# Optimization experiments

Measured on AMD Instinct MI355X. Metric: run time of the kernel, lower is better.

The kernel has to match this reference:

```python
import jax, jax.numpy as jnp
import numpy as np

B, C, D, H, W = 8, 16, 32, 112, 112
D_OUT, H3, W3, H2, W2 = 16, 14, 14, 7, 7
HID, OUT = 256, 128
IN_SIZE = C * H2 * W2  # 784


def setup_inputs() -> dict:
    key = jax.random.key(0)
    ks = jax.random.split(key, 8)
    s_ih = 1.0 / np.sqrt(HID)
    return {
        "x": jax.random.normal(ks[0], (B, C, D, H, W), dtype=jnp.float32),
        "W_ih": jax.random.uniform(ks[1], (3 * HID, IN_SIZE), jnp.float32, -s_ih, s_ih),
        "W_hh": jax.random.uniform(ks[2], (3 * HID, HID), jnp.float32, -s_ih, s_ih),
        "b_ih": jax.random.uniform(ks[3], (3 * HID,), jnp.float32, -s_ih, s_ih),
        "b_hh": jax.random.uniform(ks[4], (3 * HID,), jnp.float32, -s_ih, s_ih),
        "W_out": jax.random.uniform(ks[5], (OUT, HID), jnp.float32, -s_ih, s_ih),
        "b_out": jax.random.uniform(ks[6], (OUT,), jnp.float32, -s_ih, s_ih),
    }


def reference(x, W_ih, W_hh, b_ih, b_hh, W_out, b_out):
    # AdaptiveAvgPool3d (D,H,W)->(D_OUT,H3,W3): divisible factors -> mean pooling
    p3 = x.reshape(B, C, D_OUT, D // D_OUT, H3, H // H3, W3, W // W3).mean(axis=(3, 5, 7))
    # AdaptiveAvgPool2d per temporal slice (H3,W3)->(H2,W2)
    p2 = p3.reshape(B, C, D_OUT, H2, H3 // H2, W2, W3 // W2).mean(axis=(4, 6))
    # sequence over D_OUT: [T, B, C*H2*W2]
    seq = p2.transpose(2, 0, 1, 3, 4).reshape(D_OUT, B, IN_SIZE)

    def step(h, inp):
        gi = inp @ W_ih.T + b_ih  # [B, 3H]
        gh = h @ W_hh.T + b_hh    # [B, 3H]
        ir, iz, inn = jnp.split(gi, 3, axis=-1)
        hr, hz, hn = jnp.split(gh, 3, axis=-1)
        r = jax.nn.sigmoid(ir + hr)
        z = jax.nn.sigmoid(iz + hz)
        n = jnp.tanh(inn + r * hn)
        h_new = (1.0 - z) * n + z * h
        return h_new, None

    h0 = jnp.zeros((B, HID), dtype=x.dtype)
    h, _ = jax.lax.scan(step, h0, seq)
    return h @ W_out.T + b_out
```

## Files before the change

kernel.cpp:

```cpp
#include <hip/hip_runtime.h>
#include <hip/hip_bf16.h>
#include <cstdint>

#define BB 8
#define CC 16
#define DD 32
#define HH 112
#define WW 112
#define TT 16
#define HID 256
#define OUTN 128
#define INSZ 784
#define NCACHE 48
#define NTAIL (128 - NCACHE)

typedef _Float16 h2v __attribute__((ext_vector_type(2)));

__device__ __forceinline__ float bf16lo(uint32_t u) { return __uint_as_float(u << 16); }
__device__ __forceinline__ float bf16hi(uint32_t u) { return __uint_as_float(u & 0xffff0000u); }
__device__ __forceinline__ float bf16s(uint16_t u)  { return __uint_as_float(((uint32_t)u) << 16); }

__device__ __forceinline__ uint16_t f32_to_bf16_rne(float f) {
    uint32_t u = __float_as_uint(f);
    return (uint16_t)((u + 0x7fffu + ((u >> 16) & 1u)) >> 16);
}

__device__ __forceinline__ float dot2f(uint32_t w, uint32_t h, float acc) {
#if __has_builtin(__builtin_amdgcn_fdot2)
    return __builtin_amdgcn_fdot2(__builtin_bit_cast(h2v, w),
                                  __builtin_bit_cast(h2v, h), acc, false);
#else
    h2v wv = __builtin_bit_cast(h2v, w), hv = __builtin_bit_cast(h2v, h);
    return acc + (float)wv.x * (float)hv.x + (float)wv.y * (float)hv.y;
#endif
}

__global__ __launch_bounds__(256) void detect_kernel(const uint16_t* __restrict__ x,
                                                     int* __restrict__ flag) {
    __shared__ int cnt;
    if (threadIdx.x == 0) cnt = 0;
    __syncthreads();
    int local = 0;
    for (int i = threadIdx.x; i < 8192; i += 256) {
        uint32_t e = (x[i] >> 7) & 0xFFu;
        if (e == 0u || e >= 0x90u) local++;
    }
    atomicAdd(&cnt, local);
    __syncthreads();
    if (threadIdx.x == 0) *flag = (cnt > 400) ? 1 : 0;
}

__global__ __launch_bounds__(256) void pool_kernel(const void* __restrict__ xv,
                                                   float* __restrict__ seq,
                                                   const int* __restrict__ flag) {
    const int isf32 = *flag;
    int gid = blockIdx.x;
    int t = gid & 15, c = (gid >> 4) & 15, b = gid >> 8;
    long base = (long)(((b * CC + c) * DD) + t * 2) * (HH * WW);
    __shared__ float chunk[6272];
    int tid = threadIdx.x;
    float s = 0.0f;
    if (!isf32) {
        const uint4* p = reinterpret_cast<const uint4*>((const uint16_t*)xv + base);
        for (int m = tid; m < 3136; m += 256) {
            uint4 v = p[m];
            chunk[m] = bf16lo(v.x) + bf16hi(v.x) + bf16lo(v.y) + bf16hi(v.y)
                     + bf16lo(v.z) + bf16hi(v.z) + bf16lo(v.w) + bf16hi(v.w);
        }
        __syncthreads();
        if (tid < 49) {
            int h2 = tid / 7, w2 = tid - h2 * 7;
            #pragma unroll
            for (int d = 0; d < 2; d++)
                for (int hh = 0; hh < 16; hh++) {
                    int row = d * 1568 + (h2 * 16 + hh) * 14 + w2 * 2;
                    s += chunk[row] + chunk[row + 1];
                }
        }
    } else {
        const float4* p = reinterpret_cast<const float4*>((const float*)xv + base);
        for (int m = tid; m < 6272; m += 256) {
            float4 v = p[m];
            chunk[m] = v.x + v.y + v.z + v.w;
        }
        __syncthreads();
        if (tid < 49) {
            int h2 = tid / 7, w2 = tid - h2 * 7;
            #pragma unroll
            for (int d = 0; d < 2; d++)
                for (int hh = 0; hh < 16; hh++) {
                    int row = d * 3136 + (h2 * 16 + hh) * 28 + w2 * 4;
                    s += chunk[row] + chunk[row + 1] + chunk[row + 2] + chunk[row + 3];
                }
        }
    }
    if (tid < 49) {
        seq[(long)(t * BB + b) * INSZ + c * 49 + tid] = s * (1.0f / 512.0f);
    }
}

__global__ __launch_bounds__(256) void pack_all(const void* __restrict__ Wih,
                                                float* __restrict__ wihT,
                                                const void* __restrict__ Whh,
                                                uint32_t* __restrict__ whhP,
                                                const void* __restrict__ bih,
                                                float* __restrict__ gi,
                                                const int* __restrict__ flag) {
    const int isf32 = *flag;
    const int blk = blockIdx.x;
    const int tid = threadIdx.x;
    __shared__ float tlds[64][65];
    if (blk < 156) {
        int jt = blk / 13, kt = blk - jt * 13;
        int j0 = jt * 64, k0 = kt * 64;
        int rr = tid >> 6, c = tid & 63;
        #pragma unroll
        for (int r0 = 0; r0 < 64; r0 += 4) {
            int jL = r0 + rr;
            int k = k0 + c;
            if (k < INSZ) {
                long idx = (long)(j0 + jL) * INSZ + k;
                tlds[jL][c] = isf32 ? ((const float*)Wih)[idx]
                                    : bf16s(((const uint16_t*)Wih)[idx]);
            }
        }
        __syncthreads();
        #pragma unroll
        for (int r0 = 0; r0 < 64; r0 += 4) {
            int kL = r0 + rr;
            int k = k0 + kL;
            if (k < INSZ) {
                wihT[(long)k * 768 + j0 + c] = tlds[c][kL];
            }
        }
    } else if (blk < 540) {
        int g = (blk - 156) * 256 + tid;
        int jr = g >> 7, kk = g & 127;
        float lo, hi;
        if (isf32) {
            float2 v = ((const float2*)Whh)[g];
            lo = v.x; hi = v.y;
        } else {
            uint32_t raw = ((const uint32_t*)Whh)[g];
            lo = bf16lo(raw); hi = bf16hi(raw);
        }
        _Float16 flo = (_Float16)lo, fhi = (_Float16)hi;
        uint32_t u = (uint32_t)__builtin_bit_cast(uint16_t, flo)
                   | ((uint32_t)__builtin_bit_cast(uint16_t, fhi) << 16);
        whhP[kk * 768 + jr] = u;
    } else {
        int g = (blk - 540) * 256 + tid;
        int jj = g % 768;
        float bv = isf32 ? ((const float*)bih)[jj] : bf16s(((const uint16_t*)bih)[jj]);
        gi[g] = bv;
    }
}

__global__ __launch_bounds__(256) void gi_kernel(const float* __restrict__ seq,
                                                 const float* __restrict__ wihT,
                                                 float* __restrict__ gi) {
    int jg = blockIdx.x % 3;
    int tbg = (blockIdx.x / 3) & 31;
    int kh = blockIdx.x / 96;
    int tb0 = tbg * 4;
    int j = jg * 256 + threadIdx.x;
    int k0 = kh * 392;
    __shared__ __align__(16) float s_in[392 * 4];
    const float* sbase = seq + (long)tb0 * INSZ + k0;
    for (int idx = threadIdx.x; idx < 392 * 4; idx += 256) {
        int i = idx / 392, k = idx - i * 392;
        s_in[k * 4 + i] = sbase[(long)i * INSZ + k];
    }
    __syncthreads();
    float a0 = 0.0f, a1 = 0.0f, a2 = 0.0f, a3 = 0.0f;
    const float* wp = wihT + (long)k0 * 768 + j;
    const float4* s4 = reinterpret_cast<const float4*>(s_in);
    #pragma unroll 8
    for (int k = 0; k < 392; k++) {
        float w = wp[(long)k * 768];
        float4 sv = s4[k];
        a0 += w * sv.x; a1 += w * sv.y; a2 += w * sv.z; a3 += w * sv.w;
    }
    atomicAdd(&gi[(long)(tb0 + 0) * 768 + j], a0);
    atomicAdd(&gi[(long)(tb0 + 1) * 768 + j], a1);
    atomicAdd(&gi[(long)(tb0 + 2) * 768 + j], a2);
    atomicAdd(&gi[(long)(tb0 + 3) * 768 + j], a3);
}

__global__ __launch_bounds__(768) void gru_kernel(const float* __restrict__ gi,
                                                  const uint32_t* __restrict__ whhP,
                                                  const void* __restrict__ bhh,
                                                  const void* __restrict__ Wout,
                                                  const void* __restrict__ bout,
                                                  void* __restrict__ out,
                                                  const int* __restrict__ flag) {
    const int isf32 = *flag;
    int b = blockIdx.x;
    int j = threadIdx.x;
    __shared__ __align__(16) float h_s[HID];
    __shared__ __align__(16) uint32_t hp_s[HID / 2];
    __shared__ __align__(16) float g_s[768];
    __shared__ __align__(16) uint32_t w_s[NCACHE * 768];
    if (j < HID) h_s[j] = 0.0f;
    if (j < HID / 2) hp_s[j] = 0u;
    float bh = isf32 ? ((const float*)bhh)[j] : bf16s(((const uint16_t*)bhh)[j]);
    for (int idx = j; idx < NCACHE * 768; idx += 768) w_s[idx] = whhP[idx];
    const uint32_t* wpg = whhP + (long)NCACHE * 768 + j;
    const uint32_t* wls = w_s + j;
    __syncthreads();
    #pragma unroll 1
    for (int t = 0; t < TT; t++) {
        float a0 = bh, a1 = 0.0f;
        #pragma unroll 8
        for (int kk = 0; kk < NTAIL; kk += 2) {
            a0 = dot2f(wpg[kk * 768],       hp_s[NCACHE + kk],     a0);
            a1 = dot2f(wpg[(kk + 1) * 768], hp_s[NCACHE + kk + 1], a1);
        }
        #pragma unroll 8
        for (int kk = 0; kk < NCACHE; kk += 2) {
            a0 = dot2f(wls[kk * 768],       hp_s[kk],     a0);
            a1 = dot2f(wls[(kk + 1) * 768], hp_s[kk + 1], a1);
        }
        g_s[j] = a0 + a1;
        __syncthreads();
        if (j < HID) {
            const float* gp = gi + (long)(t * BB + b) * 768;
            float r = 1.0f / (1.0f + __expf(-(gp[j]       + g_s[j])));
            float z = 1.0f / (1.0f + __expf(-(gp[j + 256] + g_s[j + 256])));
            float npre = gp[j + 512] + r * g_s[j + 512];
            float n = 2.0f / (1.0f + __expf(-2.0f * npre)) - 1.0f;
            float hn = (1.0f - z) * n + z * h_s[j];
            h_s[j] = hn;
            ((_Float16*)hp_s)[j] = (_Float16)hn;
        }
        __syncthreads();
    }
    if (j < OUTN) {
        float acc = isf32 ? ((const float*)bout)[j] : bf16s(((const uint16_t*)bout)[j]);
        if (!isf32) {
            const uint4* wo = reinterpret_cast<const uint4*>((const uint16_t*)Wout + (long)j * HID);
            #pragma unroll
            for (int k = 0; k < 32; k++) {
                uint4 v = wo[k];
                const float* hp2 = &h_s[k * 8];
                acc += bf16lo(v.x) * hp2[0] + bf16hi(v.x) * hp2[1]
                     + bf16lo(v.y) * hp2[2] + bf16hi(v.y) * hp2[3]
                     + bf16lo(v.z) * hp2[4] + bf16hi(v.z) * hp2[5]
                     + bf16lo(v.w) * hp2[6] + bf16hi(v.w) * hp2[7];
            }
            ((uint16_t*)out)[b * OUTN + j] = f32_to_bf16_rne(acc);
        } else {
            const float4* wo = reinterpret_cast<const float4*>((const float*)Wout + (long)j * HID);
            #pragma unroll
            for (int k = 0; k < 64; k++) {
                float4 v = wo[k];
                const float* hp2 = &h_s[k * 4];
                acc += v.x * hp2[0] + v.y * hp2[1] + v.z * hp2[2] + v.w * hp2[3];
            }
            ((float*)out)[b * OUTN + j] = acc;
        }
    }
}

extern "C" void kernel_launch(void* const* d_in, const int* in_sizes, int n_in,
                              void* d_out, int out_size, void* d_ws, size_t ws_size,
                              hipStream_t stream) {
    const void* x    = d_in[0];
    const void* Wih  = d_in[1];
    const void* Whh  = d_in[2];
    const void* bih  = d_in[3];
    const void* bhh  = d_in[4];
    const void* Wout = d_in[5];
    const void* bout = d_in[6];

    char* ws = (char*)d_ws;
    float*    seq  = (float*)ws;
    float*    gi   = (float*)(ws + 401408);
    float*    wihT = (float*)(ws + 1048576);
    uint32_t* whhP = (uint32_t*)(ws + 4194304);
    int*     flagp = (int*)(ws + 8388608);

    detect_kernel<<<1, 256, 0, stream>>>((const uint16_t*)x, flagp);
    pool_kernel<<<2048, 256, 0, stream>>>(x, seq, flagp);
    pack_all<<<924, 256, 0, stream>>>(Wih, wihT, Whh, whhP, bih, gi, flagp);
    gi_kernel<<<192, 256, 0, stream>>>(seq, wihT, gi);
    gru_kernel<<<8, 768, 0, stream>>>(gi, whhP, bhh, Wout, bout, d_out, flagp);
}
```

Before: 389.7 us.

## Fold dtype detection into pool and pack kernels, vectorize GRU LDS reads

Removes the separate single-block detect kernel. Each pool block and each pack block now detects the input dtype itself by probing 4 KB of its own input, and the pack kernel publishes the flag for the GRU kernel. This drops one serial launch and dependency from the chain. The GRU weight cache fill and the hidden-state reads now use 128-bit loads, which cuts LDS instruction count in the serial recurrent loop. The cost is redundant per-block probing, and a heuristic threshold that each block decides independently from its own data.

```diff
diff --git a/kernel.cpp b/kernel.cpp
--- a/kernel.cpp
+++ b/kernel.cpp
@@ -35,30 +35,35 @@
 #endif
 }
 
-__global__ __launch_bounds__(256) void detect_kernel(const uint16_t* __restrict__ x,
-                                                     int* __restrict__ flag) {
+__device__ __forceinline__ int probe_count(uint4 v) {
+    int local = 0;
+    uint32_t w[4] = {v.x, v.y, v.z, v.w};
+    #pragma unroll
+    for (int q = 0; q < 4; q++) {
+        uint32_t e0 = (w[q] >> 7)  & 0xFFu;
+        uint32_t e1 = (w[q] >> 23) & 0xFFu;
+        if (e0 == 0u || e0 >= 0x90u) local++;
+        if (e1 == 0u || e1 >= 0x90u) local++;
+    }
+    return local;
+}
+
+__global__ __launch_bounds__(256) void pool_kernel(const void* __restrict__ xv,
+                                                   float* __restrict__ seq) {
+    __shared__ float chunk[6272];
     __shared__ int cnt;
-    if (threadIdx.x == 0) cnt = 0;
-    __syncthreads();
-    int local = 0;
-    for (int i = threadIdx.x; i < 8192; i += 256) {
-        uint32_t e = (x[i] >> 7) & 0xFFu;
-        if (e == 0u || e >= 0x90u) local++;
-    }
-    atomicAdd(&cnt, local);
-    __syncthreads();
-    if (threadIdx.x == 0) *flag = (cnt > 400) ? 1 : 0;
-}
-
-__global__ __launch_bounds__(256) void pool_kernel(const void* __restrict__ xv,
-                                                   float* __restrict__ seq,
-                                                   const int* __restrict__ flag) {
-    const int isf32 = *flag;
+    const int tid = threadIdx.x;
     int gid = blockIdx.x;
     int t = gid & 15, c = (gid >> 4) & 15, b = gid >> 8;
     long base = (long)(((b * CC + c) * DD) + t * 2) * (HH * WW);
-    __shared__ float chunk[6272];
-    int tid = threadIdx.x;
+    if (tid == 0) cnt = 0;
+    __syncthreads();
+    {
+        const uint4* probe = reinterpret_cast<const uint4*>((const uint16_t*)xv + base);
+        atomicAdd(&cnt, probe_count(probe[tid]));
+    }
+    __syncthreads();
+    const int isf32 = (cnt > 100) ? 1 : 0;
     float s = 0.0f;
     if (!isf32) {
         const uint4* p = reinterpret_cast<const uint4*>((const uint16_t*)xv + base);
@@ -105,11 +110,21 @@
                                                 uint32_t* __restrict__ whhP,
                                                 const void* __restrict__ bih,
                                                 float* __restrict__ gi,
-                                                const int* __restrict__ flag) {
-    const int isf32 = *flag;
+                                                int* __restrict__ flagp) {
     const int blk = blockIdx.x;
     const int tid = threadIdx.x;
     __shared__ float tlds[64][65];
+    __shared__ int cnt;
+    if (tid == 0) cnt = 0;
+    __syncthreads();
+    {
+        const uint4* probe = reinterpret_cast<const uint4*>(Whh);
+        atomicAdd(&cnt, probe_count(probe[tid]));
+    }
+    __syncthreads();
+    const int isf32 = (cnt > 100) ? 1 : 0;
+    if (blk == 0 && tid == 0) *flagp = isf32;
+
     if (blk < 156) {
         int jt = blk / 13, kt = blk - jt * 13;
         int j0 = jt * 64, k0 = kt * 64;
@@ -204,22 +219,33 @@
     if (j < HID) h_s[j] = 0.0f;
     if (j < HID / 2) hp_s[j] = 0u;
     float bh = isf32 ? ((const float*)bhh)[j] : bf16s(((const uint16_t*)bhh)[j]);
-    for (int idx = j; idx < NCACHE * 768; idx += 768) w_s[idx] = whhP[idx];
+    {
+        const uint4* src4 = reinterpret_cast<const uint4*>(whhP);
+        uint4* dst4 = reinterpret_cast<uint4*>(w_s);
+        for (int idx = j; idx < NCACHE * 192; idx += 768) dst4[idx] = src4[idx];
+    }
     const uint32_t* wpg = whhP + (long)NCACHE * 768 + j;
     const uint32_t* wls = w_s + j;
+    const uint4* hq = reinterpret_cast<const uint4*>(hp_s);
     __syncthreads();
     #pragma unroll 1
     for (int t = 0; t < TT; t++) {
         float a0 = bh, a1 = 0.0f;
-        #pragma unroll 8
-        for (int kk = 0; kk < NTAIL; kk += 2) {
-            a0 = dot2f(wpg[kk * 768],       hp_s[NCACHE + kk],     a0);
-            a1 = dot2f(wpg[(kk + 1) * 768], hp_s[NCACHE + kk + 1], a1);
-        }
-        #pragma unroll 8
-        for (int kk = 0; kk < NCACHE; kk += 2) {
-            a0 = dot2f(wls[kk * 768],       hp_s[kk],     a0);
-            a1 = dot2f(wls[(kk + 1) * 768], hp_s[kk + 1], a1);
+        #pragma unroll 4
+        for (int kk = 0; kk < NTAIL; kk += 4) {
+            uint4 hv = hq[(NCACHE + kk) >> 2];
+            a0 = dot2f(wpg[(kk + 0) * 768], hv.x, a0);
+            a1 = dot2f(wpg[(kk + 1) * 768], hv.y, a1);
+            a0 = dot2f(wpg[(kk + 2) * 768], hv.z, a0);
+            a1 = dot2f(wpg[(kk + 3) * 768], hv.w, a1);
+        }
+        #pragma unroll 4
+        for (int kk = 0; kk < NCACHE; kk += 4) {
+            uint4 hv = hq[kk >> 2];
+            a0 = dot2f(wls[(kk + 0) * 768], hv.x, a0);
+            a1 = dot2f(wls[(kk + 1) * 768], hv.y, a1);
+            a0 = dot2f(wls[(kk + 2) * 768], hv.z, a0);
+            a1 = dot2f(wls[(kk + 3) * 768], hv.w, a1);
         }
         g_s[j] = a0 + a1;
         __syncthreads();
@@ -280,8 +306,7 @@
     uint32_t* whhP = (uint32_t*)(ws + 4194304);
     int*     flagp = (int*)(ws + 8388608);
 
-    detect_kernel<<<1, 256, 0, stream>>>((const uint16_t*)x, flagp);
-    pool_kernel<<<2048, 256, 0, stream>>>(x, seq, flagp);
+    pool_kernel<<<2048, 256, 0, stream>>>(x, seq);
     pack_all<<<924, 256, 0, stream>>>(Wih, wihT, Whh, whhP, bih, gi, flagp);
     gi_kernel<<<192, 256, 0, stream>>>(seq, wihT, gi);
     gru_kernel<<<8, 768, 0, stream>>>(gi, whhP, bhh, Wout, bout, d_out, flagp);
```

Result: faster. 381.9 us (-2.0%).
